# Performance work log

Measured on AMD Instinct MI355X. Metric: run time of the kernel, lower is better.

Reference implementation:

```python
import jax, jax.numpy as jnp
import numpy as np

D_MODEL = 1024
NUM_HEADS = 16
D_K = D_MODEL // NUM_HEADS
THETA = 10000.0


def _rope(x, pos):
    # x: [B, H, T, d_k], pos: [T]
    inv_freq = 1.0 / (THETA ** (jnp.arange(0, D_K, 2, dtype=jnp.float32) / D_K))  # [d_k/2]
    ang = pos.astype(jnp.float32)[:, None] * inv_freq[None, :]                    # [T, d_k/2]
    cos = jnp.repeat(jnp.cos(ang), 2, axis=-1)                                    # [T, d_k]
    sin = jnp.repeat(jnp.sin(ang), 2, axis=-1)
    x = x.astype(jnp.float32)
    x0 = x[..., ::2]
    x1 = x[..., 1::2]
    rot = jnp.stack((-x1, x0), axis=-1).reshape(x.shape)  # rotate_half, interleaved
    return x * cos + rot * sin


def setup_inputs() -> dict:
    key = jax.random.key(0)
    k1, k2, k3 = jax.random.split(key, 3)
    B, T = 2, 2048
    sigma_qkv = float(np.sqrt(2.0 / (D_MODEL + 3 * D_MODEL)))
    sigma_out = float(np.sqrt(2.0 / (D_MODEL + D_MODEL)))
    return {
        "x": jax.random.normal(k1, (B, T, D_MODEL), dtype=jnp.float32),
        "w_qkv": jax.random.normal(k2, (3 * D_MODEL, D_MODEL), dtype=jnp.float32) * sigma_qkv,
        "w_out": jax.random.normal(k3, (D_MODEL, D_MODEL), dtype=jnp.float32) * sigma_out,
    }


def reference(x, w_qkv, w_out):
    B, T, _ = x.shape
    qkv = jnp.einsum("btd,ed->bte", x, w_qkv)                 # [B, T, 3*D]
    q, k, v = jnp.split(qkv, 3, axis=-1)

    def split_head(t):
        return t.reshape(B, T, NUM_HEADS, D_K).transpose(0, 2, 1, 3)  # [B, H, T, d_k]

    q, k, v = split_head(q), split_head(k), split_head(v)
    pos = jnp.arange(T)
    q = _rope(q, pos)
    k = _rope(k, pos)

    scores = jnp.einsum("bhqd,bhkd->bhqk", q, k) / jnp.sqrt(jnp.float32(D_K))
    causal = jnp.tril(jnp.ones((T, T), dtype=bool))            # True = keep
    scores = jnp.where(causal[None, None], scores, -jnp.inf)
    attn = jax.nn.softmax(scores, axis=-1)
    out = jnp.einsum("bhqk,bhkd->bhqd", attn, v)               # [B, H, T, d_k]
    out = out.transpose(0, 2, 1, 3).reshape(B, T, D_MODEL)
    return jnp.einsum("btd,ed->bte", out, w_out)
```

## Files before the change

kernel.cpp:

```cpp
#include <hip/hip_runtime.h>
#include <cstdint>
#include <cstddef>

#define BB 2
#define TT 2048
#define DMODEL 1024
#define NHEADS 16
#define DK 64

typedef short short8 __attribute__((ext_vector_type(8)));
typedef unsigned short ushort8 __attribute__((ext_vector_type(8)));
typedef float floatx4 __attribute__((ext_vector_type(4)));
typedef _Float16 half4 __attribute__((ext_vector_type(4)));

#define MFMA_PV(A, B, C) __builtin_amdgcn_mfma_f32_16x16x16f16(A, B, C, 0, 0, 0)

__device__ __forceinline__ unsigned short f2bf(float f) {
    uint32_t u = __builtin_bit_cast(uint32_t, f);
    uint32_t r = (u + 0x7FFFu + ((u >> 16) & 1u)) >> 16;
    return (unsigned short)r;
}

#define GLDS16(g, l) __builtin_amdgcn_global_load_lds( \
    (const __attribute__((address_space(1))) void*)(g), \
    (__attribute__((address_space(3))) void*)(l), 16, 0, 0)

__global__ void castk3(const float* __restrict__ x, unsigned short* __restrict__ xb,
                       const float* __restrict__ wq, unsigned short* __restrict__ wqb,
                       const float* __restrict__ wo, unsigned short* __restrict__ wob) {
    int bid = blockIdx.x;
    const float* in;
    unsigned short* out;
    int base;
    if (bid < 4096)       { in = x;  out = xb;  base = bid * 1024; }
    else if (bid < 7168)  { in = wq; out = wqb; base = (bid - 4096) * 1024; }
    else                  { in = wo; out = wob; base = (bid - 7168) * 1024; }
    int i = base + threadIdx.x * 4;
    float4 v = *(const float4*)(in + i);
    ushort4 o;
    o.x = f2bf(v.x); o.y = f2bf(v.y); o.z = f2bf(v.z); o.w = f2bf(v.w);
    *(ushort4*)(out + i) = o;
}

__global__ __launch_bounds__(256)
void gemm_bt(const unsigned short* __restrict__ A, const unsigned short* __restrict__ B,
             float* __restrict__ C, int M, int N, int K) {
    __shared__ unsigned short As[128 * 32];
    __shared__ unsigned short Bs[128 * 32];

    const int tid  = threadIdx.x;
    const int lane = tid & 63;
    const int w    = tid >> 6;
    const int wm   = w & 1;
    const int wn   = w >> 1;
    const int quad = lane >> 4;
    const int l16  = lane & 15;

    const int m0 = blockIdx.y * 128;
    const int n0 = blockIdx.x * 128;

    floatx4 acc[4][4];
#pragma unroll
    for (int a = 0; a < 4; a++)
#pragma unroll
        for (int b = 0; b < 4; b++)
            acc[a][b] = (floatx4){0.f, 0.f, 0.f, 0.f};

    const int c0 = w * 128 + lane;
    const int c1 = c0 + 64;
    const int r0 = c0 >> 2, cc0 = (c0 & 3) ^ ((r0 >> 1) & 3);
    const int r1 = c1 >> 2, cc1 = (c1 & 3) ^ ((r1 >> 1) & 3);

    const unsigned short* gA0 = A + (size_t)(m0 + r0) * K + cc0 * 8;
    const unsigned short* gA1 = A + (size_t)(m0 + r1) * K + cc1 * 8;
    const unsigned short* gB0 = B + (size_t)(n0 + r0) * K + cc0 * 8;
    const unsigned short* gB1 = B + (size_t)(n0 + r1) * K + cc1 * 8;

    unsigned short* lA0 = &As[(2 * w + 0) * 512];
    unsigned short* lA1 = &As[(2 * w + 1) * 512];
    unsigned short* lB0 = &Bs[(2 * w + 0) * 512];
    unsigned short* lB1 = &Bs[(2 * w + 1) * 512];

    const int rsw = (l16 >> 1) & 3;

    for (int k0 = 0; k0 < K; k0 += 32) {
        __syncthreads();
        GLDS16(gA0 + k0, lA0);
        GLDS16(gA1 + k0, lA1);
        GLDS16(gB0 + k0, lB0);
        GLDS16(gB1 + k0, lB1);
        __syncthreads();

        short8 af[4], bf[4];
#pragma unroll
        for (int t = 0; t < 4; t++) {
            af[t] = *(const short8*)&As[(wm * 64 + t * 16 + l16) * 32 + (quad ^ rsw) * 8];
            bf[t] = *(const short8*)&Bs[(wn * 64 + t * 16 + l16) * 32 + (quad ^ rsw) * 8];
        }
#pragma unroll
        for (int tm = 0; tm < 4; tm++)
#pragma unroll
            for (int tn = 0; tn < 4; tn++)
                acc[tm][tn] = __builtin_amdgcn_mfma_f32_16x16x32_bf16(
                    af[tm], bf[tn], acc[tm][tn], 0, 0, 0);
    }

#pragma unroll
    for (int tm = 0; tm < 4; tm++) {
#pragma unroll
        for (int tn = 0; tn < 4; tn++) {
#pragma unroll
            for (int r = 0; r < 4; r++) {
                int m = m0 + wm * 64 + tm * 16 + quad * 4 + r;
                int n = n0 + wn * 64 + tn * 16 + l16;
                C[(size_t)m * N + n] = acc[tm][tn][r];
            }
        }
    }
}

__global__ void rope_split(const float* __restrict__ qkv,
                           unsigned short* __restrict__ qb, unsigned short* __restrict__ kb) {
    int idx = blockIdx.x * blockDim.x + threadIdx.x;
    int p = idx & 31;
    int h = (idx >> 5) & 15;
    int t = (idx >> 9) & 2047;
    int b = idx >> 20;

    size_t src = (size_t)(b * TT + t) * 3072 + h * 64 + 2 * p;
    float2 q = *(const float2*)(qkv + src);
    float2 k = *(const float2*)(qkv + src + 1024);

    float invf = __powf(10000.f, -((float)(2 * p)) / 64.f);
    float ang  = (float)t * invf;
    float sn, cs;
    __sincosf(ang, &sn, &cs);

    const float QS = 0.18033688f;
    size_t dst = ((size_t)(b * NHEADS + h) * TT + t) * 64 + 2 * p;
    ushort2 qo, ko;
    qo.x = f2bf((q.x * cs - q.y * sn) * QS); qo.y = f2bf((q.y * cs + q.x * sn) * QS);
    ko.x = f2bf(k.x * cs - k.y * sn); ko.y = f2bf(k.y * cs + k.x * sn);
    *(ushort2*)(qb + dst) = qo;
    *(ushort2*)(kb + dst) = ko;
}

__global__ __launch_bounds__(256)
void vtrans(const float* __restrict__ qkv, unsigned short* __restrict__ vtb) {
    __shared__ float tile[64][65];
    const int tid = threadIdx.x;
    const int bh = blockIdx.y;
    const int b = bh >> 4, h = bh & 15;
    const int t0 = blockIdx.x * 64;

    const int row = tid >> 2;
    const float* src = qkv + ((size_t)(b * TT) + t0 + row) * 3072 + 2048 + h * 64;
#pragma unroll
    for (int i = 0; i < 4; i++) {
        int c4 = (tid & 3) * 4 + i;
        float4 v = *(const float4*)(src + c4 * 4);
        tile[row][c4 * 4 + 0] = v.x;
        tile[row][c4 * 4 + 1] = v.y;
        tile[row][c4 * 4 + 2] = v.z;
        tile[row][c4 * 4 + 3] = v.w;
    }
    __syncthreads();

    const int d  = tid >> 2;
    const int tc = tid & 3;
    const int hs = (d & 1) * 4;
    ushort8 o0, o1;
#pragma unroll
    for (int i = 0; i < 8; i++) {
        _Float16 hv = (_Float16)tile[tc * 16 + (i ^ hs)][d];
        o0[i] = __builtin_bit_cast(unsigned short, hv);
    }
#pragma unroll
    for (int i = 0; i < 8; i++) {
        _Float16 hv = (_Float16)tile[tc * 16 + 8 + (i ^ hs)][d];
        o1[i] = __builtin_bit_cast(unsigned short, hv);
    }
    unsigned short* dst = vtb + ((size_t)bh * 64 + d) * TT + t0 + tc * 16;
    *(ushort8*)(dst) = o0;
    *(ushort8*)(dst + 8) = o1;
}

__global__ __launch_bounds__(256, 5)
void attn_mfma(const unsigned short* __restrict__ qb,
               const unsigned short* __restrict__ kb,
               const unsigned short* __restrict__ vtb,
               unsigned short* __restrict__ out) {
    __shared__ unsigned short Ks[2][64 * 64];
    __shared__ unsigned short Vs[2][64 * 64];

    const int tid  = threadIdx.x;
    const int lane = tid & 63;
    const int w    = tid >> 6;
    const int quad = lane >> 4;
    const int l16  = lane & 15;

    const int bh    = blockIdx.x;
    const int qtile = gridDim.y - 1 - blockIdx.y;
    const int q0    = qtile * 64;

    const unsigned short* Qp = qb + ((size_t)bh * TT + q0 + w * 16) * 64;
    const unsigned short* Kp = kb + (size_t)bh * TT * 64;
    const unsigned short* Vp = vtb + (size_t)bh * 64 * TT;

    short8 aq[2];
#pragma unroll
    for (int ks = 0; ks < 2; ks++)
        aq[ks] = *(const short8*)(Qp + (size_t)l16 * 64 + ks * 32 + quad * 8);

    floatx4 Oacc[4];
#pragma unroll
    for (int dt = 0; dt < 4; dt++) Oacc[dt] = (floatx4){0.f, 0.f, 0.f, 0.f};
    float m = -1e30f, l = 0.f;

    const int ntiles = qtile + 1;

#define STAGE(IT, P)                                                                      \
    {                                                                                     \
        const int j0s = (IT) * 64;                                                        \
        _Pragma("unroll")                                                                 \
        for (int rep = 0; rep < 2; rep++) {                                               \
            int c    = rep * 256 + tid;                                                   \
            int row  = c >> 3, sl = c & 7;                                                \
            GLDS16(Kp + (size_t)(j0s + row) * 64 + (sl ^ (row & 7)) * 8, &Ks[P][c * 8]);  \
            GLDS16(Vp + (size_t)row * TT + j0s + (sl ^ ((row >> 1) & 7)) * 8,             \
                   &Vs[P][c * 8]);                                                        \
        }                                                                                 \
    }

    STAGE(0, 0);
    __syncthreads();

    const int ksw = l16 & 7;
    const int vsw = (l16 >> 1) & 7;
    const int vsub = ((quad & 1) ^ (l16 & 1)) * 4;

    for (int it = 0; it < ntiles; ++it) {
        const int p = it & 1;
        if (it + 1 < ntiles) STAGE(it + 1, p ^ 1);

        floatx4 sacc[4];
#pragma unroll
        for (int nt = 0; nt < 4; nt++) sacc[nt] = (floatx4){0.f, 0.f, 0.f, 0.f};
#pragma unroll
        for (int ks = 0; ks < 2; ks++)
#pragma unroll
            for (int nt = 0; nt < 4; nt++) {
                short8 kf = *(const short8*)&Ks[p][(nt * 16 + l16) * 64 + ((ks * 4 + quad) ^ ksw) * 8];
                sacc[nt] = __builtin_amdgcn_mfma_f32_16x16x32_bf16(kf, aq[ks], sacc[nt], 0, 0, 0);
            }

        if (it == qtile) {
            const int qg = w * 16 + l16;
#pragma unroll
            for (int nt = 0; nt < 4; nt++)
#pragma unroll
                for (int r = 0; r < 4; r++)
                    if (nt * 16 + quad * 4 + r > qg) sacc[nt][r] = -1e30f;
        }

        float mx = sacc[0][0];
#pragma unroll
        for (int nt = 0; nt < 4; nt++)
#pragma unroll
            for (int r = 0; r < 4; r++) mx = fmaxf(mx, sacc[nt][r]);
        mx = fmaxf(mx, __shfl_xor(mx, 16));
        mx = fmaxf(mx, __shfl_xor(mx, 32));
        float mnew  = fmaxf(m, mx);
        float alpha = __builtin_amdgcn_exp2f(m - mnew);
        m = mnew;
        float psum = 0.f;
#pragma unroll
        for (int nt = 0; nt < 4; nt++)
#pragma unroll
            for (int r = 0; r < 4; r++) {
                float pv = __builtin_amdgcn_exp2f(sacc[nt][r] - mnew);
                sacc[nt][r] = pv;
                psum += pv;
            }
        psum += __shfl_xor(psum, 16);
        psum += __shfl_xor(psum, 32);
        l = l * alpha + psum;

#pragma unroll
        for (int dt = 0; dt < 4; dt++)
#pragma unroll
            for (int r = 0; r < 4; r++) Oacc[dt][r] *= alpha;

        half4 bp[4];
#pragma unroll
        for (int nt = 0; nt < 4; nt++) {
            half4 h;
            h[0] = (_Float16)sacc[nt][0];
            h[1] = (_Float16)sacc[nt][1];
            h[2] = (_Float16)sacc[nt][2];
            h[3] = (_Float16)sacc[nt][3];
            bp[nt] = h;
        }

#pragma unroll
        for (int dt = 0; dt < 4; dt++)
#pragma unroll
            for (int nt = 0; nt < 4; nt++) {
                int c = nt * 2 + (quad >> 1);
                half4 vf = *(const half4*)&Vs[p][(dt * 16 + l16) * 64 + (c ^ vsw) * 8 + vsub];
                Oacc[dt] = MFMA_PV(vf, bp[nt], Oacc[dt]);
            }

        __syncthreads();
    }
#undef STAGE

    const int b = bh >> 4, h = bh & 15;
    const float inv = 1.f / l;
    const size_t base = ((size_t)(b * TT + q0 + w * 16 + l16)) * DMODEL + h * 64 + quad * 4;
#pragma unroll
    for (int dt = 0; dt < 4; dt++) {
        ushort4 pk;
        pk.x = f2bf(Oacc[dt][0] * inv);
        pk.y = f2bf(Oacc[dt][1] * inv);
        pk.z = f2bf(Oacc[dt][2] * inv);
        pk.w = f2bf(Oacc[dt][3] * inv);
        *(ushort4*)(out + base + dt * 16) = pk;
    }
}

extern "C" void kernel_launch(void* const* d_in, const int* in_sizes, int n_in,
                              void* d_out, int out_size, void* d_ws, size_t ws_size,
                              hipStream_t stream) {
    const float* x     = (const float*)d_in[0];
    const float* w_qkv = (const float*)d_in[1];
    const float* w_out = (const float*)d_in[2];
    float* out = (float*)d_out;

    char* ws = (char*)d_ws;

    unsigned short* xb   = (unsigned short*)(ws);
    unsigned short* wqb  = (unsigned short*)(ws + 8388608);
    unsigned short* wob  = (unsigned short*)(ws + 14680064);
    float*          qkv  = (float*)(ws + 16777216);
    unsigned short* qb   = (unsigned short*)(ws + 67108864);
    unsigned short* kb   = (unsigned short*)(ws + 75497472);
    unsigned short* vtb  = (unsigned short*)(ws + 83886080);
    unsigned short* attb = (unsigned short*)(ws + 92274688);

    castk3<<<8192, 256, 0, stream>>>(x, xb, w_qkv, wqb, w_out, wob);

    gemm_bt<<<dim3(3072 / 128, 4096 / 128), 256, 0, stream>>>(xb, wqb, qkv, 4096, 3072, 1024);

    rope_split<<<(BB * TT * NHEADS * 32) / 256, 256, 0, stream>>>(qkv, qb, kb);
    vtrans<<<dim3(TT / 64, BB * NHEADS), 256, 0, stream>>>(qkv, vtb);

    attn_mfma<<<dim3(BB * NHEADS, TT / 64), 256, 0, stream>>>(qb, kb, vtb, attb);

    gemm_bt<<<dim3(1024 / 128, 4096 / 128), 256, 0, stream>>>(attb, wob, out, 4096, 1024, 1024);
}
```

Baseline: 201.3 us.

## Double GEMM K-tile to 64 and fuse RoPE with V transpose kernel

The GEMM now stages 64-wide K slices into shared memory with an 8-way XOR swizzle and runs two MFMA k-steps per barrier pair. This halves the number of sync rounds per output tile. The RoPE/split kernel is merged into the V-transpose kernel, so one launch handles Q, K rotation and V transposition for each (batch, head, 64-token) block, removing a kernel launch. Shared memory use per GEMM block doubles, which may lower occupancy, and the loads are still not double-buffered.

```diff
diff --git a/kernel.cpp b/kernel.cpp
--- a/kernel.cpp
+++ b/kernel.cpp
@@ -45,8 +45,8 @@
 __global__ __launch_bounds__(256)
 void gemm_bt(const unsigned short* __restrict__ A, const unsigned short* __restrict__ B,
              float* __restrict__ C, int M, int N, int K) {
-    __shared__ unsigned short As[128 * 32];
-    __shared__ unsigned short Bs[128 * 32];
+    __shared__ unsigned short As[128 * 64];
+    __shared__ unsigned short Bs[128 * 64];
 
     const int tid  = threadIdx.x;
     const int lane = tid & 63;
@@ -66,43 +66,42 @@
         for (int b = 0; b < 4; b++)
             acc[a][b] = (floatx4){0.f, 0.f, 0.f, 0.f};
 
-    const int c0 = w * 128 + lane;
-    const int c1 = c0 + 64;
-    const int r0 = c0 >> 2, cc0 = (c0 & 3) ^ ((r0 >> 1) & 3);
-    const int r1 = c1 >> 2, cc1 = (c1 & 3) ^ ((r1 >> 1) & 3);
-
-    const unsigned short* gA0 = A + (size_t)(m0 + r0) * K + cc0 * 8;
-    const unsigned short* gA1 = A + (size_t)(m0 + r1) * K + cc1 * 8;
-    const unsigned short* gB0 = B + (size_t)(n0 + r0) * K + cc0 * 8;
-    const unsigned short* gB1 = B + (size_t)(n0 + r1) * K + cc1 * 8;
-
-    unsigned short* lA0 = &As[(2 * w + 0) * 512];
-    unsigned short* lA1 = &As[(2 * w + 1) * 512];
-    unsigned short* lB0 = &Bs[(2 * w + 0) * 512];
-    unsigned short* lB1 = &Bs[(2 * w + 1) * 512];
-
-    const int rsw = (l16 >> 1) & 3;
-
-    for (int k0 = 0; k0 < K; k0 += 32) {
+    int srow[4], scol[4];
+#pragma unroll
+    for (int rep = 0; rep < 4; rep++) {
+        int c = rep * 256 + tid;
+        srow[rep] = c >> 3;
+        scol[rep] = ((c & 7) ^ (srow[rep] & 7)) * 8;
+    }
+
+    const int fsw = l16 & 7;
+
+    for (int k0 = 0; k0 < K; k0 += 64) {
         __syncthreads();
-        GLDS16(gA0 + k0, lA0);
-        GLDS16(gA1 + k0, lA1);
-        GLDS16(gB0 + k0, lB0);
-        GLDS16(gB1 + k0, lB1);
+#pragma unroll
+        for (int rep = 0; rep < 4; rep++) {
+            int c = rep * 256 + tid;
+            GLDS16(A + (size_t)(m0 + srow[rep]) * K + k0 + scol[rep], &As[c * 8]);
+            GLDS16(B + (size_t)(n0 + srow[rep]) * K + k0 + scol[rep], &Bs[c * 8]);
+        }
         __syncthreads();
 
-        short8 af[4], bf[4];
-#pragma unroll
-        for (int t = 0; t < 4; t++) {
-            af[t] = *(const short8*)&As[(wm * 64 + t * 16 + l16) * 32 + (quad ^ rsw) * 8];
-            bf[t] = *(const short8*)&Bs[(wn * 64 + t * 16 + l16) * 32 + (quad ^ rsw) * 8];
-        }
-#pragma unroll
-        for (int tm = 0; tm < 4; tm++)
-#pragma unroll
-            for (int tn = 0; tn < 4; tn++)
-                acc[tm][tn] = __builtin_amdgcn_mfma_f32_16x16x32_bf16(
-                    af[tm], bf[tn], acc[tm][tn], 0, 0, 0);
+        short8 af[2][4], bf[2][4];
+#pragma unroll
+        for (int ks = 0; ks < 2; ks++)
+#pragma unroll
+            for (int t = 0; t < 4; t++) {
+                af[ks][t] = *(const short8*)&As[(wm * 64 + t * 16 + l16) * 64 + ((ks * 4 + quad) ^ fsw) * 8];
+                bf[ks][t] = *(const short8*)&Bs[(wn * 64 + t * 16 + l16) * 64 + ((ks * 4 + quad) ^ fsw) * 8];
+            }
+#pragma unroll
+        for (int ks = 0; ks < 2; ks++)
+#pragma unroll
+            for (int tm = 0; tm < 4; tm++)
+#pragma unroll
+                for (int tn = 0; tn < 4; tn++)
+                    acc[tm][tn] = __builtin_amdgcn_mfma_f32_16x16x32_bf16(
+                        af[ks][tm], bf[ks][tn], acc[tm][tn], 0, 0, 0);
     }
 
 #pragma unroll
@@ -119,39 +118,40 @@
     }
 }
 
-__global__ void rope_split(const float* __restrict__ qkv,
-                           unsigned short* __restrict__ qb, unsigned short* __restrict__ kb) {
-    int idx = blockIdx.x * blockDim.x + threadIdx.x;
-    int p = idx & 31;
-    int h = (idx >> 5) & 15;
-    int t = (idx >> 9) & 2047;
-    int b = idx >> 20;
-
-    size_t src = (size_t)(b * TT + t) * 3072 + h * 64 + 2 * p;
-    float2 q = *(const float2*)(qkv + src);
-    float2 k = *(const float2*)(qkv + src + 1024);
-
-    float invf = __powf(10000.f, -((float)(2 * p)) / 64.f);
-    float ang  = (float)t * invf;
-    float sn, cs;
-    __sincosf(ang, &sn, &cs);
-
-    const float QS = 0.18033688f;
-    size_t dst = ((size_t)(b * NHEADS + h) * TT + t) * 64 + 2 * p;
-    ushort2 qo, ko;
-    qo.x = f2bf((q.x * cs - q.y * sn) * QS); qo.y = f2bf((q.y * cs + q.x * sn) * QS);
-    ko.x = f2bf(k.x * cs - k.y * sn); ko.y = f2bf(k.y * cs + k.x * sn);
-    *(ushort2*)(qb + dst) = qo;
-    *(ushort2*)(kb + dst) = ko;
-}
-
 __global__ __launch_bounds__(256)
-void vtrans(const float* __restrict__ qkv, unsigned short* __restrict__ vtb) {
+void ropevt(const float* __restrict__ qkv,
+            unsigned short* __restrict__ qb, unsigned short* __restrict__ kb,
+            unsigned short* __restrict__ vtb) {
     __shared__ float tile[64][65];
     const int tid = threadIdx.x;
-    const int bh = blockIdx.y;
+    const int bh  = blockIdx.y;
     const int b = bh >> 4, h = bh & 15;
     const int t0 = blockIdx.x * 64;
+
+    const float QS = 0.18033688f;
+#pragma unroll
+    for (int rep = 0; rep < 8; rep++) {
+        int idx  = rep * 256 + tid;
+        int p    = idx & 31;
+        int trow = idx >> 5;
+        int t    = t0 + trow;
+
+        size_t src = (size_t)(b * TT + t) * 3072 + h * 64 + 2 * p;
+        float2 q = *(const float2*)(qkv + src);
+        float2 k = *(const float2*)(qkv + src + 1024);
+
+        float invf = __powf(10000.f, -((float)(2 * p)) / 64.f);
+        float ang  = (float)t * invf;
+        float sn, cs;
+        __sincosf(ang, &sn, &cs);
+
+        size_t dst = ((size_t)bh * TT + t) * 64 + 2 * p;
+        ushort2 qo, ko;
+        qo.x = f2bf((q.x * cs - q.y * sn) * QS); qo.y = f2bf((q.y * cs + q.x * sn) * QS);
+        ko.x = f2bf(k.x * cs - k.y * sn); ko.y = f2bf(k.y * cs + k.x * sn);
+        *(ushort2*)(qb + dst) = qo;
+        *(ushort2*)(kb + dst) = ko;
+    }
 
     const int row = tid >> 2;
     const float* src = qkv + ((size_t)(b * TT) + t0 + row) * 3072 + 2048 + h * 64;
@@ -352,8 +352,7 @@
 
     gemm_bt<<<dim3(3072 / 128, 4096 / 128), 256, 0, stream>>>(xb, wqb, qkv, 4096, 3072, 1024);
 
-    rope_split<<<(BB * TT * NHEADS * 32) / 256, 256, 0, stream>>>(qkv, qb, kb);
-    vtrans<<<dim3(TT / 64, BB * NHEADS), 256, 0, stream>>>(qkv, vtb);
+    ropevt<<<dim3(TT / 64, BB * NHEADS), 256, 0, stream>>>(qkv, qb, kb, vtb);
 
     attn_mfma<<<dim3(BB * NHEADS, TT / 64), 256, 0, stream>>>(qb, kb, vtb, attb);
 
```

Measured after the change: 195.8 us. -2.7%, faster.

## Store QKV projection in bf16 and fuse RoPE with V transpose

Applied to the files above, without the earlier changes.

The QKV GEMM now writes its output as bf16 instead of fp32, which halves the intermediate write and the reads that follow. The separate rope_split and vtrans kernels are merged into one ropevt kernel that reads the bf16 QKV buffer, so one launch is removed. The cost is an extra bf16 rounding of q, k and v before RoPE and before the fp16 V conversion, which slightly reduces precision. The GEMM epilogue still writes scalar 2-byte values, so those stores are uncoalesced in granularity.

```diff
diff --git a/kernel.cpp b/kernel.cpp
--- a/kernel.cpp
+++ b/kernel.cpp
@@ -19,6 +19,10 @@
     uint32_t u = __builtin_bit_cast(uint32_t, f);
     uint32_t r = (u + 0x7FFFu + ((u >> 16) & 1u)) >> 16;
     return (unsigned short)r;
+}
+__device__ __forceinline__ float bf2f(unsigned short s) {
+    uint32_t u = ((uint32_t)s) << 16;
+    return __builtin_bit_cast(float, u);
 }
 
 #define GLDS16(g, l) __builtin_amdgcn_global_load_lds( \
@@ -42,9 +46,10 @@
     *(ushort4*)(out + i) = o;
 }
 
+template <typename OUT>
 __global__ __launch_bounds__(256)
 void gemm_bt(const unsigned short* __restrict__ A, const unsigned short* __restrict__ B,
-             float* __restrict__ C, int M, int N, int K) {
+             OUT* __restrict__ C, int M, int N, int K) {
     __shared__ unsigned short As[128 * 32];
     __shared__ unsigned short Bs[128 * 32];
 
@@ -113,56 +118,62 @@
             for (int r = 0; r < 4; r++) {
                 int m = m0 + wm * 64 + tm * 16 + quad * 4 + r;
                 int n = n0 + wn * 64 + tn * 16 + l16;
-                C[(size_t)m * N + n] = acc[tm][tn][r];
+                if constexpr (sizeof(OUT) == 4)
+                    C[(size_t)m * N + n] = acc[tm][tn][r];
+                else
+                    C[(size_t)m * N + n] = f2bf(acc[tm][tn][r]);
             }
         }
     }
 }
 
-__global__ void rope_split(const float* __restrict__ qkv,
-                           unsigned short* __restrict__ qb, unsigned short* __restrict__ kb) {
-    int idx = blockIdx.x * blockDim.x + threadIdx.x;
-    int p = idx & 31;
-    int h = (idx >> 5) & 15;
-    int t = (idx >> 9) & 2047;
-    int b = idx >> 20;
-
-    size_t src = (size_t)(b * TT + t) * 3072 + h * 64 + 2 * p;
-    float2 q = *(const float2*)(qkv + src);
-    float2 k = *(const float2*)(qkv + src + 1024);
-
-    float invf = __powf(10000.f, -((float)(2 * p)) / 64.f);
-    float ang  = (float)t * invf;
-    float sn, cs;
-    __sincosf(ang, &sn, &cs);
-
-    const float QS = 0.18033688f;
-    size_t dst = ((size_t)(b * NHEADS + h) * TT + t) * 64 + 2 * p;
-    ushort2 qo, ko;
-    qo.x = f2bf((q.x * cs - q.y * sn) * QS); qo.y = f2bf((q.y * cs + q.x * sn) * QS);
-    ko.x = f2bf(k.x * cs - k.y * sn); ko.y = f2bf(k.y * cs + k.x * sn);
-    *(ushort2*)(qb + dst) = qo;
-    *(ushort2*)(kb + dst) = ko;
-}
-
 __global__ __launch_bounds__(256)
-void vtrans(const float* __restrict__ qkv, unsigned short* __restrict__ vtb) {
-    __shared__ float tile[64][65];
+void ropevt(const unsigned short* __restrict__ qkv,
+            unsigned short* __restrict__ qb, unsigned short* __restrict__ kb,
+            unsigned short* __restrict__ vtb) {
+    __shared__ unsigned short tile[64][72];
     const int tid = threadIdx.x;
-    const int bh = blockIdx.y;
+    const int bh  = blockIdx.y;
     const int b = bh >> 4, h = bh & 15;
     const int t0 = blockIdx.x * 64;
 
+    const float QS = 0.18033688f;
+#pragma unroll
+    for (int rep = 0; rep < 8; rep++) {
+        int idx  = rep * 256 + tid;
+        int p    = idx & 31;
+        int trow = idx >> 5;
+        int t    = t0 + trow;
+
+        size_t src = (size_t)(b * TT + t) * 3072 + h * 64 + 2 * p;
+        ushort2 qu = *(const ushort2*)(qkv + src);
+        ushort2 ku = *(const ushort2*)(qkv + src + 1024);
+        float qx = bf2f(qu.x), qy = bf2f(qu.y);
+        float kx = bf2f(ku.x), ky = bf2f(ku.y);
+
+        float invf = __powf(10000.f, -((float)(2 * p)) / 64.f);
+        float ang  = (float)t * invf;
+        float sn, cs;
+        __sincosf(ang, &sn, &cs);
+
+        size_t dst = ((size_t)bh * TT + t) * 64 + 2 * p;
+        ushort2 qo, ko;
+        qo.x = f2bf((qx * cs - qy * sn) * QS); qo.y = f2bf((qy * cs + qx * sn) * QS);
+        ko.x = f2bf(kx * cs - ky * sn); ko.y = f2bf(ky * cs + kx * sn);
+        *(ushort2*)(qb + dst) = qo;
+        *(ushort2*)(kb + dst) = ko;
+    }
+
     const int row = tid >> 2;
-    const float* src = qkv + ((size_t)(b * TT) + t0 + row) * 3072 + 2048 + h * 64;
-#pragma unroll
-    for (int i = 0; i < 4; i++) {
-        int c4 = (tid & 3) * 4 + i;
-        float4 v = *(const float4*)(src + c4 * 4);
-        tile[row][c4 * 4 + 0] = v.x;
-        tile[row][c4 * 4 + 1] = v.y;
-        tile[row][c4 * 4 + 2] = v.z;
-        tile[row][c4 * 4 + 3] = v.w;
+    const unsigned short* src = qkv + ((size_t)(b * TT) + t0 + row) * 3072 + 2048 + h * 64;
+    {
+        int cb = (tid & 3) * 16;
+        ushort8 v0 = *(const ushort8*)(src + cb);
+        ushort8 v1 = *(const ushort8*)(src + cb + 8);
+#pragma unroll
+        for (int i = 0; i < 8; i++) tile[row][cb + i] = v0[i];
+#pragma unroll
+        for (int i = 0; i < 8; i++) tile[row][cb + 8 + i] = v1[i];
     }
     __syncthreads();
 
@@ -172,12 +183,12 @@
     ushort8 o0, o1;
 #pragma unroll
     for (int i = 0; i < 8; i++) {
-        _Float16 hv = (_Float16)tile[tc * 16 + (i ^ hs)][d];
+        _Float16 hv = (_Float16)bf2f(tile[tc * 16 + (i ^ hs)][d]);
         o0[i] = __builtin_bit_cast(unsigned short, hv);
     }
 #pragma unroll
     for (int i = 0; i < 8; i++) {
-        _Float16 hv = (_Float16)tile[tc * 16 + 8 + (i ^ hs)][d];
+        _Float16 hv = (_Float16)bf2f(tile[tc * 16 + 8 + (i ^ hs)][d]);
         o1[i] = __builtin_bit_cast(unsigned short, hv);
     }
     unsigned short* dst = vtb + ((size_t)bh * 64 + d) * TT + t0 + tc * 16;
@@ -342,20 +353,21 @@
     unsigned short* xb   = (unsigned short*)(ws);
     unsigned short* wqb  = (unsigned short*)(ws + 8388608);
     unsigned short* wob  = (unsigned short*)(ws + 14680064);
-    float*          qkv  = (float*)(ws + 16777216);
-    unsigned short* qb   = (unsigned short*)(ws + 67108864);
-    unsigned short* kb   = (unsigned short*)(ws + 75497472);
-    unsigned short* vtb  = (unsigned short*)(ws + 83886080);
-    unsigned short* attb = (unsigned short*)(ws + 92274688);
+    unsigned short* qkvb = (unsigned short*)(ws + 16777216);
+    unsigned short* qb   = (unsigned short*)(ws + 41943040);
+    unsigned short* kb   = (unsigned short*)(ws + 50331648);
+    unsigned short* vtb  = (unsigned short*)(ws + 58720256);
+    unsigned short* attb = (unsigned short*)(ws + 67108864);
 
     castk3<<<8192, 256, 0, stream>>>(x, xb, w_qkv, wqb, w_out, wob);
 
-    gemm_bt<<<dim3(3072 / 128, 4096 / 128), 256, 0, stream>>>(xb, wqb, qkv, 4096, 3072, 1024);
-
-    rope_split<<<(BB * TT * NHEADS * 32) / 256, 256, 0, stream>>>(qkv, qb, kb);
-    vtrans<<<dim3(TT / 64, BB * NHEADS), 256, 0, stream>>>(qkv, vtb);
+    gemm_bt<unsigned short><<<dim3(3072 / 128, 4096 / 128), 256, 0, stream>>>(
+        xb, wqb, qkvb, 4096, 3072, 1024);
+
+    ropevt<<<dim3(TT / 64, BB * NHEADS), 256, 0, stream>>>(qkvb, qb, kb, vtb);
 
     attn_mfma<<<dim3(BB * NHEADS, TT / 64), 256, 0, stream>>>(qb, kb, vtb, attb);
 
-    gemm_bt<<<dim3(1024 / 128, 4096 / 128), 256, 0, stream>>>(attb, wob, out, 4096, 1024, 1024);
-}
+    gemm_bt<float><<<dim3(1024 / 128, 4096 / 128), 256, 0, stream>>>(
+        attb, wob, out, 4096, 1024, 1024);
+}
```

Result: faster. 191.7 us (-4.8%).
